# Kernel tuning notes

Measured on AMD Instinct MI355X. Metric: run time of the kernel, lower is better.

## Reference

```python
import jax, jax.numpy as jnp
import numpy as np

B, T, D, H, Dh, ROT = 2, 2048, 2048, 16, 128, 64
DFF = 4 * D
EPS = 1e-5
NEG = -1e9


def setup_inputs() -> dict:
    key = jax.random.key(0)
    ks = jax.random.split(key, 8)
    s = lambda k, shape, sc: jax.random.normal(k, shape, jnp.float32) * sc
    return {
        "x": s(ks[0], (B, T, D), 1.0),
        "ln_scale": jnp.ones((D,), jnp.float32),
        "ln_offset": jnp.zeros((D,), jnp.float32),
        "wq": s(ks[1], (D, D), 0.02),
        "wk": s(ks[2], (D, D), 0.02),
        "wv": s(ks[3], (D, D), 0.02),
        "wo": s(ks[4], (D, D), 0.02),
        "w1": s(ks[5], (D, DFF), 0.02),
        "b1": jnp.zeros((DFF,), jnp.float32),
        "w2": s(ks[6], (DFF, D), 0.02),
        "b2": jnp.zeros((D,), jnp.float32),
    }


def reference(x, ln_scale, ln_offset, wq, wk, wv, wo, w1, b1, w2, b2):
    def ln(h):  # ReplicatedLayerNorm, fp32 internal; note: same params used twice (shared self.norm)
        h32 = h.astype(jnp.float32)
        m = jnp.mean(h32, axis=-1, keepdims=True)
        v = jnp.var(h32, axis=-1, keepdims=True)
        y = (h32 - m) * jax.lax.rsqrt(v + EPS)
        return (y * ln_scale + ln_offset).astype(h.dtype)

    xn = ln(x)
    q = (xn @ wq).reshape(B, T, H, Dh)
    k = (xn @ wk).reshape(B, T, H, Dh)
    v = (xn @ wv).reshape(B, T, H, Dh)

    # GPT-J interleaved RoPE on first ROT dims
    pos = jnp.arange(T, dtype=jnp.float32)
    inv_freq = 1.0 / (10000.0 ** (jnp.arange(0, ROT, 2, dtype=jnp.float32) / ROT))
    freqs = pos[:, None] * inv_freq[None, :]            # (T, ROT/2)
    cos = jnp.repeat(jnp.cos(freqs), 2, axis=-1)[None, :, None, :]  # (1,T,1,ROT)
    sin = jnp.repeat(jnp.sin(freqs), 2, axis=-1)[None, :, None, :]

    def rope(t):
        tr, tp = t[..., :ROT], t[..., ROT:]
        x1 = tr[..., 0::2]
        x2 = tr[..., 1::2]
        rot_half = jnp.stack((-x2, x1), axis=-1).reshape(tr.shape)
        return jnp.concatenate([tr * cos + rot_half * sin, tp], axis=-1)

    q, k = rope(q), rope(k)

    scale = 1.0 / jnp.sqrt(jnp.float32(Dh))
    scores = jnp.einsum('bthd,bshd->bhts', q, k) * scale
    mask = jnp.where(jnp.tril(jnp.ones((T, T), bool)), 0.0, NEG).astype(scores.dtype)
    w = jax.nn.softmax(scores + mask, axis=-1)
    ctx = jnp.einsum('bhts,bshd->bthd', w, v).reshape(B, T, D)
    x1_ = x + ctx @ wo

    xn2 = ln(x1_)
    h = jax.nn.gelu(xn2.astype(jnp.float32) @ w1 + b1)  # default approximate gelu, as in source
    ff = (h @ w2 + b2).astype(x.dtype)
    return x1_ + ff
```

## Files before the change

### kernel.cpp

```cpp
#include <hip/hip_runtime.h>
#include <hip/hip_bf16.h>

#define B_   2
#define T_   2048
#define D_   2048
#define H_   16
#define DH_  128
#define DFF_ 8192

typedef __attribute__((ext_vector_type(8))) short bf16x8;
typedef __attribute__((ext_vector_type(4))) float f32x4;

__device__ __forceinline__ short f2bf(float f) {
    __hip_bfloat16 h = __float2bfloat16(f);
    return *reinterpret_cast<short*>(&h);
}

__device__ __forceinline__ void gload_lds16(const void* g, void* l) {
    __builtin_amdgcn_global_load_lds(
        (const __attribute__((address_space(1))) void*)g,
        (__attribute__((address_space(3))) void*)l,
        16, 0, 0);
}

__device__ __forceinline__ float gelu_tanh(float x) {
    float x3 = x * x * x;
    return 0.5f * x * (1.f + tanhf(0.7978845608028654f * (x + 0.044715f * x3)));
}

#define MFMA32(a, b, c) __builtin_amdgcn_mfma_f32_16x16x32_bf16((a), (b), (c), 0, 0, 0)

__global__ __launch_bounds__(256) void transpose_cvt(const float* __restrict__ in,
                                                     __hip_bfloat16* __restrict__ out,
                                                     int K, int N, int out_ld, int out_row0)
{
    __shared__ float t[32][65];
    const int n0 = blockIdx.x * 64, k0 = blockIdx.y * 32;
    const int tid = threadIdx.x;
    {
        int kr = tid >> 4;
        int nc = (tid & 15) * 4;
        const float* src = in + (size_t)(k0 + kr) * N + n0 + nc;
        float4 a = *reinterpret_cast<const float4*>(src);
        float4 b = *reinterpret_cast<const float4*>(src + (size_t)16 * N);
        t[kr][nc] = a.x; t[kr][nc + 1] = a.y; t[kr][nc + 2] = a.z; t[kr][nc + 3] = a.w;
        t[kr + 16][nc] = b.x; t[kr + 16][nc + 1] = b.y; t[kr + 16][nc + 2] = b.z; t[kr + 16][nc + 3] = b.w;
    }
    __syncthreads();
    {
        int n  = tid >> 2;
        int kc = (tid & 3) * 8;
        __hip_bfloat16 ob[8];
#pragma unroll
        for (int j = 0; j < 8; ++j) ob[j] = __float2bfloat16(t[kc + j][n]);
        *reinterpret_cast<uint4*>(out + (size_t)(out_row0 + n0 + n) * out_ld + k0 + kc) =
            *reinterpret_cast<uint4*>(ob);
    }
}

__global__ __launch_bounds__(256) void ln_kernel(const float* __restrict__ x,
                                                 const float* __restrict__ sc,
                                                 const float* __restrict__ of,
                                                 __hip_bfloat16* __restrict__ out)
{
    int row = blockIdx.x, tid = threadIdx.x;
    const float* xr = x + (size_t)row * D_;
    float4 v0 = reinterpret_cast<const float4*>(xr)[tid * 2];
    float4 v1 = reinterpret_cast<const float4*>(xr)[tid * 2 + 1];
    float vv[8] = {v0.x, v0.y, v0.z, v0.w, v1.x, v1.y, v1.z, v1.w};
    float s = 0.f, ss = 0.f;
#pragma unroll
    for (int j = 0; j < 8; ++j) { s += vv[j]; ss += vv[j] * vv[j]; }
    for (int o = 32; o; o >>= 1) { s += __shfl_down(s, o); ss += __shfl_down(ss, o); }
    __shared__ float red[8];
    int wid = tid >> 6, lane = tid & 63;
    if (!lane) { red[wid] = s; red[4 + wid] = ss; }
    __syncthreads();
    s  = red[0] + red[1] + red[2] + red[3];
    ss = red[4] + red[5] + red[6] + red[7];
    float mean = s * (1.f / D_);
    float var  = ss * (1.f / D_) - mean * mean;
    float rstd = rsqrtf(var + 1e-5f);
    int c0 = tid * 8;
    __hip_bfloat16 ob[8];
#pragma unroll
    for (int j = 0; j < 8; ++j)
        ob[j] = __float2bfloat16((vv[j] - mean) * rstd * sc[c0 + j] + of[c0 + j]);
    *reinterpret_cast<uint4*>(out + (size_t)row * D_ + c0) = *reinterpret_cast<uint4*>(ob);
}

template<int EPI>
__global__ __launch_bounds__(512, 4) void gemmq(
    const __hip_bfloat16* __restrict__ A, const __hip_bfloat16* __restrict__ BT,
    void* __restrict__ Cout, const float* __restrict__ bias,
    const float* __restrict__ resid, int M, int N, int K)
{
    __shared__ short As[2 * 2 * 128 * 32];
    __shared__ short Bs[2 * 2 * 128 * 32];

    const int tid = threadIdx.x;
    const int wid = tid >> 6, lane = tid & 63;
    const int lo = lane & 15, hi = lane >> 4;
    const int wr = wid >> 2, wc = wid & 3;

    const int gx = gridDim.x;
    const int nwg = gx * gridDim.y;
    const int bid = blockIdx.y * gx + blockIdx.x;
    const int swz = (bid & 7) * (nwg >> 3) + (bid >> 3);
    const int m0 = (swz / gx) * 128, n0 = (swz % gx) * 128;

    const int srow = tid >> 2, sslot = tid & 3;
    auto stageA = [&](int tt, int ks) {
        int kc = tt * 64 + ks * 32 + ((sslot ^ ((srow >> 1) & 3)) << 3);
        gload_lds16(A + (size_t)(m0 + srow) * K + kc,
                    (char*)As + ((tt & 1) * 2 + ks) * 8192 + wid * 1024);
    };
    auto stageB = [&](int tt, int ks) {
        int kc = tt * 64 + ks * 32 + ((sslot ^ ((srow >> 1) & 3)) << 3);
        gload_lds16(BT + (size_t)(n0 + srow) * K + kc,
                    (char*)Bs + ((tt & 1) * 2 + ks) * 8192 + wid * 1024);
    };

    const int fsw  = (hi ^ ((lo >> 1) & 3)) << 4;
    const int arow = wr * 64 + lo;
    const int brow = wc * 32 + lo;

    f32x4 acc[4][2] = {};
    const int NT = K >> 6;

    stageA(0, 0); stageB(0, 0); stageA(0, 1); stageB(0, 1);
    asm volatile("s_waitcnt vmcnt(2)" ::: "memory");
    __builtin_amdgcn_s_barrier();
    __builtin_amdgcn_sched_barrier(0);

#pragma unroll 2
    for (int t = 0; t < NT; ++t) {
        const int bsel = t & 1;
        const bool pf = (t + 1 < NT);
        const char* Ab = (const char*)As + bsel * 16384;
        const char* Bb = (const char*)Bs + bsel * 16384;

#pragma unroll
        for (int ks = 0; ks < 2; ++ks) {
            bf16x8 af[4], b0, b1;
#pragma unroll
            for (int m = 0; m < 4; ++m)
                af[m] = *reinterpret_cast<const bf16x8*>(
                    Ab + ks * 8192 + (arow + m * 16) * 64 + fsw);
            b0 = *reinterpret_cast<const bf16x8*>(Bb + ks * 8192 + brow * 64 + fsw);
            b1 = *reinterpret_cast<const bf16x8*>(Bb + ks * 8192 + (brow + 16) * 64 + fsw);
            if (pf) { stageA(t + 1, ks); stageB(t + 1, ks); }
            asm volatile("s_waitcnt lgkmcnt(0)" ::: "memory");
            __builtin_amdgcn_sched_barrier(0);
            __builtin_amdgcn_s_setprio(1);
#pragma unroll
            for (int m = 0; m < 4; ++m) {
                acc[m][0] = MFMA32(af[m], b0, acc[m][0]);
                acc[m][1] = MFMA32(af[m], b1, acc[m][1]);
            }
            __builtin_amdgcn_s_setprio(0);
            if (pf) asm volatile("s_waitcnt vmcnt(2)" ::: "memory");
            else    asm volatile("s_waitcnt vmcnt(0)" ::: "memory");
            __builtin_amdgcn_s_barrier();
            __builtin_amdgcn_sched_barrier(0);
        }
    }

    float* Cf = (float*)Cout;
    __hip_bfloat16* Cb = (__hip_bfloat16*)Cout;

    bool doRope = false;
    float invf[2];
    if (EPI == 4) {
        doRope = (n0 < 4096) && (wc < 2);
        if (doRope) {
#pragma unroll
            for (int j = 0; j < 2; ++j) {
                int p = (wc * 32 + j * 16 + lo) >> 1;
                invf[j] = exp2f((float)p * -0.4152410118609203f);
            }
        }
    }

#pragma unroll
    for (int m = 0; m < 4; ++m) {
        int rbase = m0 + wr * 64 + m * 16 + hi * 4;
#pragma unroll
        for (int j = 0; j < 2; ++j) {
            int col = n0 + wc * 32 + j * 16 + lo;
            float bv = (EPI == 2 || EPI == 3) ? bias[col] : 0.f;
#pragma unroll
            for (int i = 0; i < 4; ++i) {
                size_t idx = (size_t)(rbase + i) * N + col;
                float v = acc[m][j][i];
                if (EPI == 4) {
                    if (doRope) {
                        float pv = __shfl_xor(v, 1);
                        int tt = (rbase + i) & (T_ - 1);
                        float fr = (float)tt * invf[j];
                        float cs, sn;
                        __sincosf(fr, &sn, &cs);
                        v = (lo & 1) ? (v * cs + pv * sn) : (v * cs - pv * sn);
                    }
                    Cb[idx] = __float2bfloat16(v);
                    continue;
                }
                if (EPI == 2 || EPI == 3) v += bv;
                if (EPI == 2) v = gelu_tanh(v);
                if (EPI == 1 || EPI == 3) v += resid[idx];
                if (EPI == 0 || EPI == 2) Cb[idx] = __float2bfloat16(v);
                else                      Cf[idx] = v;
            }
        }
    }
}

__global__ __launch_bounds__(512) void attn_kernel(const __hip_bfloat16* __restrict__ qkv,
                                                   __hip_bfloat16* __restrict__ ctx)
{
    constexpr int LDQ = 3 * D_;
    constexpr int SV  = 68;

    int idx = blockIdx.y * 16 + blockIdx.x;
    int swz = (idx & 7) * 64 + (idx >> 3);
    const int bh  = swz >> 4;
    const int bxr = 15 - (swz & 15);
    const int b = bh >> 4, h = bh & 15;
    const int tq0 = bxr * 128;

    const int tid = threadIdx.x, wid = tid >> 6, lane = tid & 63;
    const int lo = lane & 15, hi = lane >> 4;
    const int t0 = tq0 + wid * 16;

    __shared__ short Ks[2][64 * 128];
    __shared__ short VsT[128 * SV];

    const __hip_bfloat16* qrow = qkv + (size_t)(b * T_ + t0 + lo) * LDQ + h * DH_;
    bf16x8 qf[4];
#pragma unroll
    for (int dk = 0; dk < 4; ++dk)
        qf[dk] = *reinterpret_cast<const bf16x8*>(qrow + dk * 32 + hi * 8);

    f32x4 octx[8] = {};
    float mreg = -1e30f, lreg = 0.f;

    const size_t kvrow0 = (size_t)(b * T_) * LDQ + h * DH_;
    const int nst = 2 * (bxr + 1);

    bf16x8 vr[2];

#define STAGE_K(s0v, buf)                                                     \
    do {                                                                      \
        _Pragma("unroll")                                                     \
        for (int i = 0; i < 2; ++i) {                                         \
            int c    = i * 512 + tid;                                         \
            int sr   = c >> 4;                                                \
            int cbs  = ((c & 15) * 16) ^ ((sr & 7) << 4);                     \
            gload_lds16(qkv + kvrow0 + (size_t)((s0v) + sr) * LDQ + D_ + (cbs >> 1), \
                        &Ks[buf][c * 8]);                                     \
        }                                                                     \
    } while (0)

#define LOAD_V(s0v)                                                           \
    do {                                                                      \
        _Pragma("unroll")                                                     \
        for (int it = 0; it < 2; ++it) {                                      \
            int c = it * 512 + tid;                                           \
            int s = c >> 4, dc = c & 15;                                      \
            vr[it] = *reinterpret_cast<const bf16x8*>(                        \
                qkv + kvrow0 + (size_t)((s0v) + s) * LDQ + 2 * D_ + dc * 8);  \
        }                                                                     \
    } while (0)

    STAGE_K(0, 0);
    LOAD_V(0);

    for (int st = 0; st < nst; ++st) {
        const int s0 = st * 64;
        const int cur = st & 1;
        __syncthreads();

#pragma unroll
        for (int it = 0; it < 2; ++it) {
            int c = it * 512 + tid;
            int s = c >> 4, dc = c & 15;
            int sswz = s ^ ((dc & 15) << 2);
            short* dst = &VsT[(dc * 8) * SV + sswz];
#pragma unroll
            for (int j = 0; j < 8; ++j)
                dst[j * SV] = vr[it][j];
        }
        if (st + 1 < nst) {
            STAGE_K(s0 + 64, cur ^ 1);
            LOAD_V(s0 + 64);
        }
        asm volatile("s_waitcnt lgkmcnt(0)" ::: "memory");
        __builtin_amdgcn_s_barrier();
        __builtin_amdgcn_sched_barrier(0);

        f32x4 sfr[4] = {};
        __builtin_amdgcn_s_setprio(1);
#pragma unroll
        for (int f = 0; f < 4; ++f) {
            int srow = f * 16 + lo;
            int sw = (srow & 7) << 4;
#pragma unroll
            for (int dk = 0; dk < 4; ++dk) {
                bf16x8 kf = *reinterpret_cast<const bf16x8*>(
                    (const char*)&Ks[cur][0] + srow * 256 + ((dk * 64 + hi * 16) ^ sw));
                sfr[f] = MFMA32(kf, qf[dk], sfr[f]);
            }
        }
        __builtin_amdgcn_s_setprio(0);

        const float qsc = 0.08838834764831845f;
#pragma unroll
        for (int f = 0; f < 4; ++f)
#pragma unroll
            for (int i = 0; i < 4; ++i)
                sfr[f][i] *= qsc;
        if (st >= nst - 2) {
#pragma unroll
            for (int f = 0; f < 4; ++f)
#pragma unroll
                for (int i = 0; i < 4; ++i)
                    if (s0 + f * 16 + hi * 4 + i > t0 + lo) sfr[f][i] = -1e30f;
        }

        float mx = -1e30f;
#pragma unroll
        for (int f = 0; f < 4; ++f)
#pragma unroll
            for (int i = 0; i < 4; ++i)
                mx = fmaxf(mx, sfr[f][i]);
        mx = fmaxf(mx, __shfl_xor(mx, 16));
        mx = fmaxf(mx, __shfl_xor(mx, 32));

        if (!__all(mx - mreg <= 8.f)) {
            float mn = fmaxf(mreg, mx);
            float ps = __expf(mreg - mn);
            mreg = mn;
            lreg *= ps;
            float psq[4];
#pragma unroll
            for (int i = 0; i < 4; ++i)
                psq[i] = __shfl(ps, hi * 4 + i);
#pragma unroll
            for (int f8 = 0; f8 < 8; ++f8)
#pragma unroll
                for (int i = 0; i < 4; ++i)
                    octx[f8][i] *= psq[i];
        }

        float sum = 0.f;
#pragma unroll
        for (int f = 0; f < 4; ++f)
#pragma unroll
            for (int i = 0; i < 4; ++i) {
                sfr[f][i] = __expf(sfr[f][i] - mreg);
                sum += sfr[f][i];
            }
        sum += __shfl_xor(sum, 16);
        sum += __shfl_xor(sum, 32);
        lreg += sum;

#pragma unroll
        for (int ks = 0; ks < 2; ++ks) {
            union { bf16x8 v; short s[8]; } pa;
#pragma unroll
            for (int j = 0; j < 4; ++j) {
                pa.s[j]     = f2bf(sfr[2 * ks][j]);
                pa.s[j + 4] = f2bf(sfr[2 * ks + 1][j]);
            }
            __builtin_amdgcn_s_setprio(1);
#pragma unroll
            for (int f8 = 0; f8 < 8; ++f8) {
                int d = f8 * 16 + lo;
                int sw2 = ((d >> 3) & 15) << 2;
                const short* vrow = &VsT[d * SV];
                union { bf16x8 v; uint2 u[2]; } vb;
                vb.u[0] = *reinterpret_cast<const uint2*>(vrow + ((ks * 32 + hi * 4) ^ sw2));
                vb.u[1] = *reinterpret_cast<const uint2*>(vrow + ((ks * 32 + 16 + hi * 4) ^ sw2));
                octx[f8] = MFMA32(pa.v, vb.v, octx[f8]);
            }
            __builtin_amdgcn_s_setprio(0);
        }
    }
#undef STAGE_K
#undef LOAD_V

    float linv[4];
#pragma unroll
    for (int i = 0; i < 4; ++i)
        linv[i] = 1.f / __shfl(lreg, hi * 4 + i);
#pragma unroll
    for (int i = 0; i < 4; ++i) {
        size_t rb = (size_t)(b * T_ + t0 + hi * 4 + i) * D_ + h * DH_;
#pragma unroll
        for (int f8 = 0; f8 < 8; ++f8)
            ctx[rb + f8 * 16 + lo] = __float2bfloat16(octx[f8][i] * linv[i]);
    }
}

extern "C" void kernel_launch(void* const* d_in, const int* in_sizes, int n_in,
                              void* d_out, int out_size, void* d_ws, size_t ws_size,
                              hipStream_t stream)
{
    (void)in_sizes; (void)n_in; (void)out_size; (void)ws_size;
    const float* x   = (const float*)d_in[0];
    const float* lns = (const float*)d_in[1];
    const float* lno = (const float*)d_in[2];
    const float* wq  = (const float*)d_in[3];
    const float* wk  = (const float*)d_in[4];
    const float* wv  = (const float*)d_in[5];
    const float* wo  = (const float*)d_in[6];
    const float* w1  = (const float*)d_in[7];
    const float* b1  = (const float*)d_in[8];
    const float* w2  = (const float*)d_in[9];
    const float* b2  = (const float*)d_in[10];
    float* out = (float*)d_out;

    char* ws = (char*)d_ws;
    __hip_bfloat16* wqkvT = (__hip_bfloat16*)(ws);
    __hip_bfloat16* woT   = (__hip_bfloat16*)(ws + 25165824);
    __hip_bfloat16* w1T   = (__hip_bfloat16*)(ws + 33554432);
    __hip_bfloat16* w2T   = (__hip_bfloat16*)(ws + 67108864);
    __hip_bfloat16* xn    = (__hip_bfloat16*)(ws + 100663296);
    __hip_bfloat16* qkv   = (__hip_bfloat16*)(ws + 117440512);
    __hip_bfloat16* hbuf  = qkv;
    __hip_bfloat16* ctx   = (__hip_bfloat16*)(ws + 167772160);
    float*          x1    = (float*)(ws + 184549376);

    transpose_cvt<<<dim3(32, 64),  256, 0, stream>>>(wq, wqkvT, 2048, 2048, 2048, 0);
    transpose_cvt<<<dim3(32, 64),  256, 0, stream>>>(wk, wqkvT, 2048, 2048, 2048, 2048);
    transpose_cvt<<<dim3(32, 64),  256, 0, stream>>>(wv, wqkvT, 2048, 2048, 2048, 4096);
    transpose_cvt<<<dim3(32, 64),  256, 0, stream>>>(wo, woT,   2048, 2048, 2048, 0);
    transpose_cvt<<<dim3(128, 64), 256, 0, stream>>>(w1, w1T,   2048, 8192, 2048, 0);
    transpose_cvt<<<dim3(32, 256), 256, 0, stream>>>(w2, w2T,   8192, 2048, 8192, 0);

    ln_kernel<<<4096, 256, 0, stream>>>(x, lns, lno, xn);
    gemmq<4><<<dim3(48, 32), 512, 0, stream>>>(xn, wqkvT, qkv, nullptr, nullptr, 4096, 6144, 2048);
    attn_kernel<<<dim3(16, 32), 512, 0, stream>>>(qkv, ctx);
    gemmq<1><<<dim3(16, 32), 512, 0, stream>>>(ctx, woT, x1, nullptr, x, 4096, 2048, 2048);
    ln_kernel<<<4096, 256, 0, stream>>>(x1, lns, lno, xn);
    gemmq<2><<<dim3(64, 32), 512, 0, stream>>>(xn, w1T, hbuf, b1, nullptr, 4096, 8192, 2048);
    gemmq<3><<<dim3(16, 32), 512, 0, stream>>>(hbuf, w2T, out, b2, x1, 4096, 2048, 8192);
}
```

Measured before the change: 757.1 us.

## Add larger-tile 8-wave GEMM with split-phase prefetch for QKV and FFN1

Introduces a gemm8p kernel using 128x256 or 256x256 output tiles with four B fragments per wave. The per-K-step schedule is split into four phases that interleave A/B prefetch with MFMA batches. It is used for the QKV projection (with the RoPE epilogue adapted to the new column mapping) and the FFN1 GELU GEMM. The goal is higher arithmetic intensity per LDS byte and fewer global loads per FLOP, at the cost of more registers and LDS, lower occupancy (launch bounds 2), and fewer workgroups for the 256-CU device.

```diff
diff --git a/kernel.cpp b/kernel.cpp
--- a/kernel.cpp
+++ b/kernel.cpp
@@ -89,14 +89,17 @@
     *reinterpret_cast<uint4*>(out + (size_t)row * D_ + c0) = *reinterpret_cast<uint4*>(ob);
 }
 
-template<int EPI>
-__global__ __launch_bounds__(512, 4) void gemmq(
+template<int EPI, int BM>
+__global__ __launch_bounds__(512, 2) void gemm8p(
     const __hip_bfloat16* __restrict__ A, const __hip_bfloat16* __restrict__ BT,
     void* __restrict__ Cout, const float* __restrict__ bias,
     const float* __restrict__ resid, int M, int N, int K)
 {
-    __shared__ short As[2 * 2 * 128 * 32];
-    __shared__ short Bs[2 * 2 * 128 * 32];
+    constexpr int MFR = BM / 32;
+    constexpr int AUL = BM / 128;
+    constexpr int VMC = AUL + 2;
+    __shared__ short As[2 * 2 * BM * 32];
+    __shared__ short Bs[2 * 2 * 256 * 32];
 
     const int tid = threadIdx.x;
     const int wid = tid >> 6, lane = tid & 63;
@@ -107,87 +110,123 @@
     const int nwg = gx * gridDim.y;
     const int bid = blockIdx.y * gx + blockIdx.x;
     const int swz = (bid & 7) * (nwg >> 3) + (bid >> 3);
-    const int m0 = (swz / gx) * 128, n0 = (swz % gx) * 128;
-
-    const int srow = tid >> 2, sslot = tid & 3;
+    const int m0 = (swz / gx) * BM, n0 = (swz % gx) * 256;
+
     auto stageA = [&](int tt, int ks) {
-        int kc = tt * 64 + ks * 32 + ((sslot ^ ((srow >> 1) & 3)) << 3);
-        gload_lds16(A + (size_t)(m0 + srow) * K + kc,
-                    (char*)As + ((tt & 1) * 2 + ks) * 8192 + wid * 1024);
+#pragma unroll
+        for (int l = 0; l < AUL; ++l) {
+            int c    = l * 512 + tid;
+            int row  = c >> 2, ksub = c & 3;
+            int kc   = tt * 64 + ks * 32 + ((ksub ^ ((row >> 1) & 3)) << 3);
+            int c0   = l * 512 + wid * 64;
+            gload_lds16(A + (size_t)(m0 + row) * K + kc,
+                        (char*)As + ((tt & 1) * 2 + ks) * (BM * 64) + c0 * 16);
+        }
     };
     auto stageB = [&](int tt, int ks) {
-        int kc = tt * 64 + ks * 32 + ((sslot ^ ((srow >> 1) & 3)) << 3);
-        gload_lds16(BT + (size_t)(n0 + srow) * K + kc,
-                    (char*)Bs + ((tt & 1) * 2 + ks) * 8192 + wid * 1024);
+#pragma unroll
+        for (int l = 0; l < 2; ++l) {
+            int c    = l * 512 + tid;
+            int row  = c >> 2, ksub = c & 3;
+            int kc   = tt * 64 + ks * 32 + ((ksub ^ ((row >> 1) & 3)) << 3);
+            int c0   = l * 512 + wid * 64;
+            gload_lds16(BT + (size_t)(n0 + row) * K + kc,
+                        (char*)Bs + ((tt & 1) * 2 + ks) * 16384 + c0 * 16);
+        }
     };
 
     const int fsw  = (hi ^ ((lo >> 1) & 3)) << 4;
-    const int arow = wr * 64 + lo;
-    const int brow = wc * 32 + lo;
-
-    f32x4 acc[4][2] = {};
+    const int arow = wr * (BM / 2) + lo;
+    const int brow = wc * 64 + lo;
+
+    f32x4 acc[MFR][4] = {};
     const int NT = K >> 6;
 
     stageA(0, 0); stageB(0, 0); stageA(0, 1); stageB(0, 1);
-    asm volatile("s_waitcnt vmcnt(2)" ::: "memory");
+    asm volatile("s_waitcnt vmcnt(%0)" :: "i"(VMC) : "memory");
     __builtin_amdgcn_s_barrier();
     __builtin_amdgcn_sched_barrier(0);
+
+#define PHASE_MFMA(J)                                                         \
+        __builtin_amdgcn_s_barrier();                                         \
+        asm volatile("s_waitcnt lgkmcnt(0)" ::: "memory");                    \
+        __builtin_amdgcn_sched_barrier(0);                                    \
+        __builtin_amdgcn_s_setprio(1);                                        \
+        _Pragma("unroll")                                                     \
+        for (int m = 0; m < MFR; ++m) {                                       \
+            acc[m][J]     = MFMA32(af[m], b0, acc[m][J]);                     \
+            acc[m][J + 1] = MFMA32(af[m], b1, acc[m][J + 1]);                 \
+        }                                                                     \
+        __builtin_amdgcn_s_setprio(0);
 
 #pragma unroll 2
     for (int t = 0; t < NT; ++t) {
         const int bsel = t & 1;
         const bool pf = (t + 1 < NT);
-        const char* Ab = (const char*)As + bsel * 16384;
-        const char* Bb = (const char*)Bs + bsel * 16384;
-
-#pragma unroll
-        for (int ks = 0; ks < 2; ++ks) {
-            bf16x8 af[4], b0, b1;
-#pragma unroll
-            for (int m = 0; m < 4; ++m)
-                af[m] = *reinterpret_cast<const bf16x8*>(
-                    Ab + ks * 8192 + (arow + m * 16) * 64 + fsw);
-            b0 = *reinterpret_cast<const bf16x8*>(Bb + ks * 8192 + brow * 64 + fsw);
-            b1 = *reinterpret_cast<const bf16x8*>(Bb + ks * 8192 + (brow + 16) * 64 + fsw);
-            if (pf) { stageA(t + 1, ks); stageB(t + 1, ks); }
-            asm volatile("s_waitcnt lgkmcnt(0)" ::: "memory");
-            __builtin_amdgcn_sched_barrier(0);
-            __builtin_amdgcn_s_setprio(1);
-#pragma unroll
-            for (int m = 0; m < 4; ++m) {
-                acc[m][0] = MFMA32(af[m], b0, acc[m][0]);
-                acc[m][1] = MFMA32(af[m], b1, acc[m][1]);
-            }
-            __builtin_amdgcn_s_setprio(0);
-            if (pf) asm volatile("s_waitcnt vmcnt(2)" ::: "memory");
-            else    asm volatile("s_waitcnt vmcnt(0)" ::: "memory");
-            __builtin_amdgcn_s_barrier();
-            __builtin_amdgcn_sched_barrier(0);
-        }
-    }
+        const char* Ab = (const char*)As + bsel * (2 * BM * 64);
+        const char* Bb = (const char*)Bs + bsel * 32768;
+        bf16x8 af[MFR], b0, b1;
+
+#pragma unroll
+        for (int m = 0; m < MFR; ++m)
+            af[m] = *reinterpret_cast<const bf16x8*>(Ab + (arow + m * 16) * 64 + fsw);
+        b0 = *reinterpret_cast<const bf16x8*>(Bb + brow * 64 + fsw);
+        b1 = *reinterpret_cast<const bf16x8*>(Bb + (brow + 16) * 64 + fsw);
+        if (pf) stageA(t + 1, 0);
+        PHASE_MFMA(0)
+        __builtin_amdgcn_s_barrier();
+        __builtin_amdgcn_sched_barrier(0);
+
+        b0 = *reinterpret_cast<const bf16x8*>(Bb + (brow + 32) * 64 + fsw);
+        b1 = *reinterpret_cast<const bf16x8*>(Bb + (brow + 48) * 64 + fsw);
+        if (pf) stageB(t + 1, 0);
+        PHASE_MFMA(2)
+        asm volatile("s_waitcnt vmcnt(%0)" :: "i"(VMC) : "memory");
+        __builtin_amdgcn_s_barrier();
+        __builtin_amdgcn_sched_barrier(0);
+
+#pragma unroll
+        for (int m = 0; m < MFR; ++m)
+            af[m] = *reinterpret_cast<const bf16x8*>(Ab + BM * 64 + (arow + m * 16) * 64 + fsw);
+        b0 = *reinterpret_cast<const bf16x8*>(Bb + 16384 + brow * 64 + fsw);
+        b1 = *reinterpret_cast<const bf16x8*>(Bb + 16384 + (brow + 16) * 64 + fsw);
+        if (pf) stageA(t + 1, 1);
+        PHASE_MFMA(0)
+        __builtin_amdgcn_s_barrier();
+        __builtin_amdgcn_sched_barrier(0);
+
+        b0 = *reinterpret_cast<const bf16x8*>(Bb + 16384 + (brow + 32) * 64 + fsw);
+        b1 = *reinterpret_cast<const bf16x8*>(Bb + 16384 + (brow + 48) * 64 + fsw);
+        if (pf) stageB(t + 1, 1);
+        PHASE_MFMA(2)
+        asm volatile("s_waitcnt vmcnt(%0)" :: "i"(VMC) : "memory");
+        __builtin_amdgcn_s_barrier();
+        __builtin_amdgcn_sched_barrier(0);
+    }
+#undef PHASE_MFMA
 
     float* Cf = (float*)Cout;
     __hip_bfloat16* Cb = (__hip_bfloat16*)Cout;
 
     bool doRope = false;
-    float invf[2];
+    float invf[4];
     if (EPI == 4) {
-        doRope = (n0 < 4096) && (wc < 2);
+        doRope = (n0 < 4096) && ((wc & 1) == 0);
         if (doRope) {
 #pragma unroll
-            for (int j = 0; j < 2; ++j) {
-                int p = (wc * 32 + j * 16 + lo) >> 1;
+            for (int j = 0; j < 4; ++j) {
+                int p = ((j >> 1) * 32 + (j & 1) * 16 + lo) >> 1;
                 invf[j] = exp2f((float)p * -0.4152410118609203f);
             }
         }
     }
 
 #pragma unroll
-    for (int m = 0; m < 4; ++m) {
-        int rbase = m0 + wr * 64 + m * 16 + hi * 4;
-#pragma unroll
-        for (int j = 0; j < 2; ++j) {
-            int col = n0 + wc * 32 + j * 16 + lo;
+    for (int m = 0; m < MFR; ++m) {
+        int rbase = m0 + wr * (BM / 2) + m * 16 + hi * 4;
+#pragma unroll
+        for (int j = 0; j < 4; ++j) {
+            int col = n0 + wc * 64 + (j >> 1) * 32 + (j & 1) * 16 + lo;
             float bv = (EPI == 2 || EPI == 3) ? bias[col] : 0.f;
 #pragma unroll
             for (int i = 0; i < 4; ++i) {
@@ -215,6 +254,106 @@
     }
 }
 
+template<int EPI>
+__global__ __launch_bounds__(512, 4) void gemmq(
+    const __hip_bfloat16* __restrict__ A, const __hip_bfloat16* __restrict__ BT,
+    void* __restrict__ Cout, const float* __restrict__ bias,
+    const float* __restrict__ resid, int M, int N, int K)
+{
+    __shared__ short As[2 * 2 * 128 * 32];
+    __shared__ short Bs[2 * 2 * 128 * 32];
+
+    const int tid = threadIdx.x;
+    const int wid = tid >> 6, lane = tid & 63;
+    const int lo = lane & 15, hi = lane >> 4;
+    const int wr = wid >> 2, wc = wid & 3;
+
+    const int gx = gridDim.x;
+    const int nwg = gx * gridDim.y;
+    const int bid = blockIdx.y * gx + blockIdx.x;
+    const int swz = (bid & 7) * (nwg >> 3) + (bid >> 3);
+    const int m0 = (swz / gx) * 128, n0 = (swz % gx) * 128;
+
+    const int srow = tid >> 2, sslot = tid & 3;
+    auto stageA = [&](int tt, int ks) {
+        int kc = tt * 64 + ks * 32 + ((sslot ^ ((srow >> 1) & 3)) << 3);
+        gload_lds16(A + (size_t)(m0 + srow) * K + kc,
+                    (char*)As + ((tt & 1) * 2 + ks) * 8192 + wid * 1024);
+    };
+    auto stageB = [&](int tt, int ks) {
+        int kc = tt * 64 + ks * 32 + ((sslot ^ ((srow >> 1) & 3)) << 3);
+        gload_lds16(BT + (size_t)(n0 + srow) * K + kc,
+                    (char*)Bs + ((tt & 1) * 2 + ks) * 8192 + wid * 1024);
+    };
+
+    const int fsw  = (hi ^ ((lo >> 1) & 3)) << 4;
+    const int arow = wr * 64 + lo;
+    const int brow = wc * 32 + lo;
+
+    f32x4 acc[4][2] = {};
+    const int NT = K >> 6;
+
+    stageA(0, 0); stageB(0, 0); stageA(0, 1); stageB(0, 1);
+    asm volatile("s_waitcnt vmcnt(2)" ::: "memory");
+    __builtin_amdgcn_s_barrier();
+    __builtin_amdgcn_sched_barrier(0);
+
+#pragma unroll 2
+    for (int t = 0; t < NT; ++t) {
+        const int bsel = t & 1;
+        const bool pf = (t + 1 < NT);
+        const char* Ab = (const char*)As + bsel * 16384;
+        const char* Bb = (const char*)Bs + bsel * 16384;
+
+#pragma unroll
+        for (int ks = 0; ks < 2; ++ks) {
+            bf16x8 af[4], b0, b1;
+#pragma unroll
+            for (int m = 0; m < 4; ++m)
+                af[m] = *reinterpret_cast<const bf16x8*>(
+                    Ab + ks * 8192 + (arow + m * 16) * 64 + fsw);
+            b0 = *reinterpret_cast<const bf16x8*>(Bb + ks * 8192 + brow * 64 + fsw);
+            b1 = *reinterpret_cast<const bf16x8*>(Bb + ks * 8192 + (brow + 16) * 64 + fsw);
+            if (pf) { stageA(t + 1, ks); stageB(t + 1, ks); }
+            asm volatile("s_waitcnt lgkmcnt(0)" ::: "memory");
+            __builtin_amdgcn_sched_barrier(0);
+            __builtin_amdgcn_s_setprio(1);
+#pragma unroll
+            for (int m = 0; m < 4; ++m) {
+                acc[m][0] = MFMA32(af[m], b0, acc[m][0]);
+                acc[m][1] = MFMA32(af[m], b1, acc[m][1]);
+            }
+            __builtin_amdgcn_s_setprio(0);
+            if (pf) asm volatile("s_waitcnt vmcnt(2)" ::: "memory");
+            else    asm volatile("s_waitcnt vmcnt(0)" ::: "memory");
+            __builtin_amdgcn_s_barrier();
+            __builtin_amdgcn_sched_barrier(0);
+        }
+    }
+
+    float* Cf = (float*)Cout;
+    __hip_bfloat16* Cb = (__hip_bfloat16*)Cout;
+#pragma unroll
+    for (int m = 0; m < 4; ++m) {
+        int rbase = m0 + wr * 64 + m * 16 + hi * 4;
+#pragma unroll
+        for (int j = 0; j < 2; ++j) {
+            int col = n0 + wc * 32 + j * 16 + lo;
+            float bv = (EPI == 2 || EPI == 3) ? bias[col] : 0.f;
+#pragma unroll
+            for (int i = 0; i < 4; ++i) {
+                size_t idx = (size_t)(rbase + i) * N + col;
+                float v = acc[m][j][i];
+                if (EPI == 2 || EPI == 3) v += bv;
+                if (EPI == 2) v = gelu_tanh(v);
+                if (EPI == 1 || EPI == 3) v += resid[idx];
+                if (EPI == 0 || EPI == 2) Cb[idx] = __float2bfloat16(v);
+                else                      Cf[idx] = v;
+            }
+        }
+    }
+}
+
 __global__ __launch_bounds__(512) void attn_kernel(const __hip_bfloat16* __restrict__ qkv,
                                                    __hip_bfloat16* __restrict__ ctx)
 {
@@ -439,10 +578,10 @@
     transpose_cvt<<<dim3(32, 256), 256, 0, stream>>>(w2, w2T,   8192, 2048, 8192, 0);
 
     ln_kernel<<<4096, 256, 0, stream>>>(x, lns, lno, xn);
-    gemmq<4><<<dim3(48, 32), 512, 0, stream>>>(xn, wqkvT, qkv, nullptr, nullptr, 4096, 6144, 2048);
+    gemm8p<4, 128><<<dim3(24, 32), 512, 0, stream>>>(xn, wqkvT, qkv, nullptr, nullptr, 4096, 6144, 2048);
     attn_kernel<<<dim3(16, 32), 512, 0, stream>>>(qkv, ctx);
     gemmq<1><<<dim3(16, 32), 512, 0, stream>>>(ctx, woT, x1, nullptr, x, 4096, 2048, 2048);
     ln_kernel<<<4096, 256, 0, stream>>>(x1, lns, lno, xn);
-    gemmq<2><<<dim3(64, 32), 512, 0, stream>>>(xn, w1T, hbuf, b1, nullptr, 4096, 8192, 2048);
+    gemm8p<2, 256><<<dim3(32, 16), 512, 0, stream>>>(xn, w1T, hbuf, b1, nullptr, 4096, 8192, 2048);
     gemmq<3><<<dim3(16, 32), 512, 0, stream>>>(hbuf, w2T, out, b2, x1, 4096, 2048, 8192);
 }
```

Result: faster. 722.3 us (-4.6%).
